# Kernel optimization log

Measured on AMD Instinct MI355X. Metric: run time of the kernel, lower is better.

The kernel has to match this reference:

```python
import jax, jax.numpy as jnp
import numpy as np

B, H, W, C = 4, 48, 48, 256
NQ = 8
NH = 8
FFN = 1024


def _dwconv(x, w, b):
    # x: (b,h,w,c); w: (kh,kw,1,c) depthwise; b: (c,)
    p = w.shape[0] // 2
    y = jax.lax.conv_general_dilated(
        x, w, (1, 1), [(p, p), (p, p)],
        dimension_numbers=('NHWC', 'HWIO', 'NHWC'),
        feature_group_count=x.shape[-1])
    return y + b


def _ln(x, g, b, eps=1e-6):
    m = jnp.mean(x, -1, keepdims=True)
    v = jnp.mean((x - m) ** 2, -1, keepdims=True)
    return (x - m) * jax.lax.rsqrt(v + eps) * g + b


def setup_inputs() -> dict:
    key = jax.random.key(0)
    ks = jax.random.split(key, 16)
    s = lambda k, sh, sc=0.02: jax.random.normal(k, sh, jnp.float32) * sc
    return dict(
        x=jax.random.normal(ks[0], (B, H, W, C), jnp.float32),
        queries=jax.random.normal(ks[1], (B, NQ, C), jnp.float32),
        epoch=10,
        pos_w=s(ks[2], (3, 3, 1, C)), pos_b=jnp.zeros((C,), jnp.float32),
        ln1_g=jnp.ones((C,), jnp.float32), ln1_b=jnp.zeros((C,), jnp.float32),
        q_w=s(ks[3], (C, C)), q_b=jnp.zeros((C,), jnp.float32),
        k_w=s(ks[4], (C, C)), k_b=jnp.zeros((C,), jnp.float32),
        v_w=s(ks[5], (C, C)), v_b=jnp.zeros((C,), jnp.float32),
        lepe_w=s(ks[6], (5, 5, 1, C)), lepe_b=jnp.zeros((C,), jnp.float32),
        out_w=s(ks[7], (C, C)), out_b=jnp.zeros((C,), jnp.float32),
        ln2_g=jnp.ones((C,), jnp.float32), ln2_b=jnp.zeros((C,), jnp.float32),
        fc1_w=s(ks[8], (FFN, C)), fc1_b=jnp.zeros((FFN,), jnp.float32),
        fc2_w=s(ks[9], (C, FFN)), fc2_b=jnp.zeros((C,), jnp.float32),
    )


def reference(x, queries, epoch, pos_w, pos_b, ln1_g, ln1_b,
              q_w, q_b, k_w, k_b, v_w, v_b, lepe_w, lepe_b,
              out_w, out_b, ln2_g, ln2_b, fc1_w, fc1_b, fc2_w, fc2_b):
    b, h, w, c = x.shape
    nq = queries.shape[1]
    N = nq + h * w

    # positional DWConv (3x3) residual
    x = x + _dwconv(x, pos_w, pos_b)
    xf = x.reshape(b, h * w, c)
    xq = jnp.concatenate([queries, xf], axis=1)  # (b, N, c)

    # region mask (epoch=10 -> soft softmax phase, tau exp-decayed)
    tau = 2.0 * (0.1 / 2.0) ** (epoch / 200.0)
    logits = jnp.einsum('bnc,bqc->bnq', xf, queries)  # (b, hw, nq)
    p = jax.nn.softmax(logits / tau, axis=-1)
    region = jnp.einsum('bik,bjk->bij', p, p)  # (b, hw, hw)
    mask = jnp.ones((b, N, N), x.dtype).at[:, nq:, nq:].set(region)

    # masked attention (faithful: v_h is built from scaled k, as in source)
    y = _ln(xq, ln1_g, ln1_b)
    q = y @ q_w.T + q_b
    k = y @ k_w.T + k_b
    v = y @ v_w.T + v_b
    lepe = _dwconv(v[:, nq:].reshape(b, h, w, -1), lepe_w, lepe_b).reshape(b, h * w, -1)
    k = k * (c // NH) ** -0.5
    qh = q.reshape(b, N, NH, -1).transpose(0, 2, 1, 3)  # (b, nh, N, d)
    kh = k.reshape(b, N, NH, -1).transpose(0, 2, 1, 3)
    vh = kh  # source assigns v_h from k
    qk = jnp.einsum('bhnd,bhmd->bhnm', qh, kh) * mask[:, None]
    att = jax.nn.softmax(qk, axis=-1)
    o = jnp.einsum('bhnm,bhmd->bhnd', att, vh)
    o = o.transpose(0, 2, 1, 3).reshape(b, N, -1)
    o = o.at[:, nq:, :].add(lepe)
    o = o @ out_w.T + out_b
    xq = xq + o

    # FFN
    z = _ln(xq, ln2_g, ln2_b)
    z = jax.nn.gelu(z @ fc1_w.T + fc1_b, approximate=False)
    z = z @ fc2_w.T + fc2_b
    xq = xq + z

    return xq[:, nq:, :].reshape(b, h, w, c), xq[:, :nq, :]
```

## Files before the change

kernel.cpp:

```cpp
#include <hip/hip_runtime.h>
#include <hip/hip_bf16.h>
#include <math.h>

typedef unsigned short u16;
constexpr int Bc = 4, Hc = 48, Wc = 48, Cc = 256;
constexpr int NQc = 8, HWc = 2304, Nc = 2312, NHc = 8, Dc = 32, FFNc = 1024;
constexpr int MRc = Bc * Nc;
constexpr int KTLDc = 2368;
constexpr float KSCALEc = 0.17677669529663687f;
constexpr float LOG2Ec  = 1.4426950408889634f;

typedef __attribute__((ext_vector_type(8))) short s8v;
typedef __attribute__((ext_vector_type(4))) float f32x4;

__device__ __forceinline__ u16 f2bf(float f) {
    union { __hip_bfloat16 h; u16 u; } c;
    c.h = __float2bfloat16(f);
    return c.u;
}
__device__ __forceinline__ float bf2f(u16 u) {
    return __uint_as_float(((unsigned)u) << 16);
}
__device__ __forceinline__ unsigned cvtpk2(float lo, float hi) {
    unsigned r;
    asm("v_cvt_pk_bf16_f32 %0, %1, %2" : "=v"(r) : "v"(lo), "v"(hi));
    return r;
}
__device__ __forceinline__ float fast_exp2(float x) {
    float r;
    asm("v_exp_f32 %0, %1" : "=v"(r) : "v"(x));
    return r;
}
__device__ __forceinline__ void gload16(const void* g, void* l) {
    __builtin_amdgcn_global_load_lds((const __attribute__((address_space(1))) void*)g,
                                     (__attribute__((address_space(3))) void*)l, 16, 0, 0);
}

__global__ __launch_bounds__(256) void fused_pre_kernel(
    const float* __restrict__ x, const float* __restrict__ queries, const int* __restrict__ epoch,
    const float* __restrict__ pos_w, const float* __restrict__ pos_b,
    const float* __restrict__ ln_g, const float* __restrict__ ln_b,
    const float* __restrict__ qw, const float* __restrict__ kw, const float* __restrict__ vw,
    const float* __restrict__ ow, const float* __restrict__ f1, const float* __restrict__ f2,
    float* __restrict__ xq, u16* __restrict__ ybf, u16* __restrict__ pbf,
    u16* __restrict__ wbf, u16* __restrict__ kt)
{
    int bi = blockIdx.x;
    if (bi >= 9248) {
        int bj = bi - 9248;
        if (bj < 768) {
            int i4 = bj * 256 + threadIdx.x;
            int idx = i4 * 4;
            const float* src; int off;
            if      (idx < 65536)  { src = qw; off = idx; }
            else if (idx < 131072) { src = kw; off = idx - 65536; }
            else if (idx < 196608) { src = vw; off = idx - 131072; }
            else if (idx < 262144) { src = ow; off = idx - 196608; }
            else if (idx < 524288) { src = f1; off = idx - 262144; }
            else                   { src = f2; off = idx - 524288; }
            float4 v = *(const float4*)(src + off);
            ushort4 o;
            o.x = f2bf(v.x); o.y = f2bf(v.y); o.z = f2bf(v.z); o.w = f2bf(v.w);
            *(ushort4*)(wbf + idx) = o;
        } else {
            int idx = (bj - 768) * 256 + threadIdx.x;
            if (idx < 1024 * 56) {
                int row = idx / 56, col = idx - row * 56;
                kt[(size_t)row * KTLDc + 2312 + col] = 0;
            }
        }
        return;
    }
    int blk = bi;
    int b = blk / Nc, n = blk - b * Nc;
    int c = threadIdx.x;
    bool sp = (n >= NQc);
    float val;
    if (sp) {
        int s = n - NQc;
        int hh = s / Wc, ww = s - hh * Wc;
        float acc = pos_b[c];
        float center = x[((b * Hc + hh) * Wc + ww) * Cc + c];
#pragma unroll
        for (int kh = 0; kh < 3; ++kh) {
            int yy = hh + kh - 1;
            if (yy < 0 || yy >= Hc) continue;
#pragma unroll
            for (int kw2 = 0; kw2 < 3; ++kw2) {
                int xx = ww + kw2 - 1;
                if (xx < 0 || xx >= Wc) continue;
                acc += x[((b * Hc + yy) * Wc + xx) * Cc + c] * pos_w[(kh * 3 + kw2) * Cc + c];
            }
        }
        val = center + acc;
    } else {
        val = queries[(b * NQc + n) * Cc + c];
    }
    xq[(size_t)blk * Cc + c] = val;

    float pq[8];
#pragma unroll
    for (int qi = 0; qi < 8; ++qi)
        pq[qi] = sp ? val * queries[(b * NQc + qi) * Cc + c] : 0.f;
    float r0 = val, r1 = val * val;
#pragma unroll
    for (int off = 32; off; off >>= 1) {
        r0 += __shfl_xor(r0, off);
        r1 += __shfl_xor(r1, off);
#pragma unroll
        for (int qi = 0; qi < 8; ++qi) pq[qi] += __shfl_xor(pq[qi], off);
    }
    __shared__ float red[4][10];
    __shared__ float fin[10];
    int wv = c >> 6, ln = c & 63;
    if (ln == 0) {
        red[wv][0] = r0; red[wv][1] = r1;
#pragma unroll
        for (int qi = 0; qi < 8; ++qi) red[wv][2 + qi] = pq[qi];
    }
    __syncthreads();
    if (c < 10) fin[c] = red[0][c] + red[1][c] + red[2][c] + red[3][c];
    __syncthreads();
    float mean = fin[0] * (1.0f / 256.0f);
    float var  = fin[1] * (1.0f / 256.0f) - mean * mean;
    float inv  = rsqrtf(var + 1e-6f);
    ybf[(size_t)blk * Cc + c] = f2bf((val - mean) * inv * ln_g[c] + ln_b[c]);

    if (sp && c < 8) {
        float it = 1.0f / (2.0f * powf(0.05f, (float)(*epoch) / 200.0f));
        float mx = -1e30f;
        float lg[8];
#pragma unroll
        for (int qi = 0; qi < 8; ++qi) { lg[qi] = fin[2 + qi] * it; mx = fmaxf(mx, lg[qi]); }
        float s = 0.f, mine = 0.f;
#pragma unroll
        for (int qi = 0; qi < 8; ++qi) {
            float ev = __expf(lg[qi] - mx);
            s += ev;
            if (qi == c) mine = ev;
        }
        pbf[((size_t)b * HWc + (n - NQc)) * 8 + c] = f2bf(mine / s);
    }
}

template <int ACT, int RESID, int OMODE>
__global__ __launch_bounds__(256) void mfma_gemm64_kernel(
    const u16* __restrict__ A, const u16* __restrict__ W,
    const float* __restrict__ bias, const float* resid,
    float* outF, u16* outB, int M, int N, int K, float scale)
{
    __shared__ u16 As[64 * 64];
    __shared__ u16 Bs[128 * 64];
    int t = threadIdx.x;
    int w = t >> 6, l = t & 63, lg = l >> 4, lr = l & 15;
    int wm = w >> 1, wn = w & 1;
    int m0 = blockIdx.y * 64, n0 = blockIdx.x * 128;
    f32x4 acc[2][4] = {};
    int lrow = l >> 3, lchunk = (l & 7) * 8;
    for (int k0 = 0; k0 < K; k0 += 64) {
        __syncthreads();
#pragma unroll
        for (int c = 0; c < 2; ++c) {
            int ar = m0 + w * 16 + c * 8 + lrow;
            if (ar >= M) ar = M - 1;
            gload16(A + (size_t)ar * K + k0 + lchunk, As + (w * 16 + c * 8) * 64);
        }
#pragma unroll
        for (int c = 0; c < 4; ++c) {
            int br = n0 + w * 32 + c * 8 + lrow;
            gload16(W + (size_t)br * K + k0 + lchunk, Bs + (w * 32 + c * 8) * 64);
        }
        __syncthreads();
#pragma unroll
        for (int kk = 0; kk < 64; kk += 32) {
            s8v aF[2], bF[4];
#pragma unroll
            for (int i = 0; i < 2; ++i)
                aF[i] = *(s8v*)&As[(wm * 32 + i * 16 + lr) * 64 + kk + lg * 8];
#pragma unroll
            for (int j = 0; j < 4; ++j)
                bF[j] = *(s8v*)&Bs[(wn * 64 + j * 16 + lr) * 64 + kk + lg * 8];
#pragma unroll
            for (int i = 0; i < 2; ++i)
#pragma unroll
                for (int j = 0; j < 4; ++j)
                    acc[i][j] = __builtin_amdgcn_mfma_f32_16x16x32_bf16(aF[i], bF[j], acc[i][j], 0, 0, 0);
        }
    }
#pragma unroll
    for (int j = 0; j < 4; ++j) {
        int n = n0 + wn * 64 + j * 16 + lr;
        float bv = bias[n];
#pragma unroll
        for (int i = 0; i < 2; ++i) {
#pragma unroll
            for (int r = 0; r < 4; ++r) {
                int m = m0 + wm * 32 + i * 16 + lg * 4 + r;
                if (m >= M) continue;
                float v = (acc[i][j][r] + bv) * scale;
                if (ACT == 1) {
                    float e = fast_exp2(2.302118f * (v + 0.044715f * v * v * v));
                    v = v * e * __builtin_amdgcn_rcpf(e + 1.0f);
                }
                if (RESID) v += resid[(size_t)m * N + n];
                if (OMODE == 0) {
                    outF[(size_t)m * N + n] = v;
                } else if (OMODE == 3) {
                    unsigned bb2 = (unsigned)m / 2312u;
                    unsigned tok = (unsigned)m - bb2 * 2312u;
                    size_t ob = (tok >= 8) ? (((size_t)(bb2 * 2304 + tok - 8)) << 8)
                                           : ((size_t)2359296 + (((size_t)(bb2 * 8 + tok)) << 8));
                    outF[ob + n] = v;
                } else {
                    outB[(size_t)m * N + n] = f2bf(v);
                }
            }
        }
    }
}

__global__ __launch_bounds__(256) void mfma_gemm_oln_kernel(
    const u16* __restrict__ A, const u16* __restrict__ V,
    const float* __restrict__ lw, const float* __restrict__ lbias,
    const u16* __restrict__ W, const float* __restrict__ bias,
    float* __restrict__ xq, const float* __restrict__ g, const float* __restrict__ bb,
    u16* __restrict__ ybf)
{
    const int K = Cc;
    constexpr int ALD = 264;
    __shared__ u16 As[32 * ALD];
    __shared__ u16 Bs[256 * 64];
    __shared__ float R[32][4][2];
    __shared__ float MI[32][2];
    int t = threadIdx.x;
    int w = t >> 6, l = t & 63, lg = l >> 4, lr = l & 15;
    int m0 = blockIdx.x * 32;
    int lrow = l >> 3, lchunk = (l & 7) * 8;

    for (int u = t; u < 1024; u += 256) {
        int row = u >> 5;
        int cg  = (u & 31) * 8;
        int m = m0 + row;
        int b2 = m / 2312, n = m - b2 * 2312;
        union { s8v s; u16 us[8]; } ov, res;
        ov.s = *(const s8v*)&A[(size_t)m * Cc + cg];
        if (n >= NQc) {
            int s0 = n - NQc, hh = s0 / Wc, ww = s0 - hh * Wc;
            float accv[8];
#pragma unroll
            for (int i = 0; i < 8; ++i) accv[i] = lbias[cg + i];
#pragma unroll
            for (int kh = 0; kh < 5; ++kh) {
                int yy = hh + kh - 2;
                if (yy < 0 || yy >= Hc) continue;
#pragma unroll
                for (int kw = 0; kw < 5; ++kw) {
                    int xx = ww + kw - 2;
                    if (xx < 0 || xx >= Wc) continue;
                    union { s8v s; u16 us[8]; } uv;
                    uv.s = *(const s8v*)&V[((size_t)b2 * Nc + NQc + yy * Wc + xx) * Cc + cg];
                    const float4* wp = (const float4*)&lw[(kh * 5 + kw) * Cc + cg];
                    float4 w0 = wp[0], w1 = wp[1];
                    accv[0] += bf2f(uv.us[0]) * w0.x;
                    accv[1] += bf2f(uv.us[1]) * w0.y;
                    accv[2] += bf2f(uv.us[2]) * w0.z;
                    accv[3] += bf2f(uv.us[3]) * w0.w;
                    accv[4] += bf2f(uv.us[4]) * w1.x;
                    accv[5] += bf2f(uv.us[5]) * w1.y;
                    accv[6] += bf2f(uv.us[6]) * w1.z;
                    accv[7] += bf2f(uv.us[7]) * w1.w;
                }
            }
#pragma unroll
            for (int i = 0; i < 8; ++i) res.us[i] = f2bf(bf2f(ov.us[i]) + accv[i]);
        } else {
            res.s = ov.s;
        }
        *(s8v*)&As[row * ALD + cg] = res.s;
    }

    f32x4 acc[2][4] = {};
    for (int k0 = 0; k0 < K; k0 += 64) {
        __syncthreads();
#pragma unroll
        for (int c = 0; c < 8; ++c)
            gload16(W + (size_t)(w * 64 + c * 8 + lrow) * K + k0 + lchunk, Bs + (w * 64 + c * 8) * 64);
        __syncthreads();
#pragma unroll
        for (int kk = 0; kk < 64; kk += 32) {
            s8v aF[2], bF[4];
#pragma unroll
            for (int i = 0; i < 2; ++i)
                aF[i] = *(s8v*)&As[(i * 16 + lr) * ALD + k0 + kk + lg * 8];
#pragma unroll
            for (int j = 0; j < 4; ++j)
                bF[j] = *(s8v*)&Bs[(w * 64 + j * 16 + lr) * 64 + kk + lg * 8];
#pragma unroll
            for (int i = 0; i < 2; ++i)
#pragma unroll
                for (int j = 0; j < 4; ++j)
                    acc[i][j] = __builtin_amdgcn_mfma_f32_16x16x32_bf16(aF[i], bF[j], acc[i][j], 0, 0, 0);
        }
    }
    float s[2][4], ss[2][4];
#pragma unroll
    for (int i = 0; i < 2; ++i)
#pragma unroll
        for (int r = 0; r < 4; ++r) { s[i][r] = 0.f; ss[i][r] = 0.f; }
#pragma unroll
    for (int j = 0; j < 4; ++j) {
        int n = w * 64 + j * 16 + lr;
        float bv = bias[n];
#pragma unroll
        for (int i = 0; i < 2; ++i) {
#pragma unroll
            for (int r = 0; r < 4; ++r) {
                int m = m0 + i * 16 + lg * 4 + r;
                float v = acc[i][j][r] + bv + xq[(size_t)m * Cc + n];
                acc[i][j][r] = v;
                xq[(size_t)m * Cc + n] = v;
                s[i][r] += v;
                ss[i][r] += v * v;
            }
        }
    }
#pragma unroll
    for (int i = 0; i < 2; ++i)
#pragma unroll
        for (int r = 0; r < 4; ++r) {
#pragma unroll
            for (int off = 1; off < 16; off <<= 1) {
                s[i][r]  += __shfl_xor(s[i][r], off);
                ss[i][r] += __shfl_xor(ss[i][r], off);
            }
        }
    __syncthreads();
    if (lr == 0) {
#pragma unroll
        for (int i = 0; i < 2; ++i)
#pragma unroll
            for (int r = 0; r < 4; ++r) {
                int row = i * 16 + lg * 4 + r;
                R[row][w][0] = s[i][r];
                R[row][w][1] = ss[i][r];
            }
    }
    __syncthreads();
    if (t < 32) {
        float tot  = R[t][0][0] + R[t][1][0] + R[t][2][0] + R[t][3][0];
        float tots = R[t][0][1] + R[t][1][1] + R[t][2][1] + R[t][3][1];
        float mean = tot * (1.0f / 256.0f);
        float var  = tots * (1.0f / 256.0f) - mean * mean;
        MI[t][0] = mean;
        MI[t][1] = rsqrtf(var + 1e-6f);
    }
    __syncthreads();
#pragma unroll
    for (int j = 0; j < 4; ++j) {
        int n = w * 64 + j * 16 + lr;
        float gv = g[n], bbv = bb[n];
#pragma unroll
        for (int i = 0; i < 2; ++i) {
#pragma unroll
            for (int r = 0; r < 4; ++r) {
                int row = i * 16 + lg * 4 + r;
                float mean = MI[row][0], inv = MI[row][1];
                int m = m0 + row;
                ybf[(size_t)m * Cc + n] = f2bf((acc[i][j][r] - mean) * inv * gv + bbv);
            }
        }
    }
}

__global__ __launch_bounds__(256) void mfma_gemm_qkv64_kernel(
    const u16* __restrict__ A, const u16* __restrict__ W,
    const float* __restrict__ q_b, const float* __restrict__ k_b, const float* __restrict__ v_b,
    u16* __restrict__ outq, u16* __restrict__ outk, u16* __restrict__ outkt, u16* __restrict__ outv)
{
    const int M = MRc, K = Cc;
    __shared__ u16 As[64 * 64];
    __shared__ u16 Bs[128 * 64];
    int t = threadIdx.x;
    int w = t >> 6, l = t & 63, lg = l >> 4, lr = l & 15;
    int wm = w >> 1, wn = w & 1;
    int m0 = blockIdx.y * 64, n0 = blockIdx.x * 128;
    int range = n0 >> 8;
    f32x4 acc[2][4] = {};
    int lrow = l >> 3, lchunk = (l & 7) * 8;
    for (int k0 = 0; k0 < K; k0 += 64) {
        __syncthreads();
#pragma unroll
        for (int c = 0; c < 2; ++c) {
            int ar = m0 + w * 16 + c * 8 + lrow;
            if (ar >= M) ar = M - 1;
            gload16(A + (size_t)ar * K + k0 + lchunk, As + (w * 16 + c * 8) * 64);
        }
#pragma unroll
        for (int c = 0; c < 4; ++c) {
            int br = n0 + w * 32 + c * 8 + lrow;
            gload16(W + (size_t)br * K + k0 + lchunk, Bs + (w * 32 + c * 8) * 64);
        }
        __syncthreads();
#pragma unroll
        for (int kk = 0; kk < 64; kk += 32) {
            s8v aF[2], bF[4];
#pragma unroll
            for (int i = 0; i < 2; ++i)
                aF[i] = *(s8v*)&As[(wm * 32 + i * 16 + lr) * 64 + kk + lg * 8];
#pragma unroll
            for (int j = 0; j < 4; ++j)
                bF[j] = *(s8v*)&Bs[(wn * 64 + j * 16 + lr) * 64 + kk + lg * 8];
#pragma unroll
            for (int i = 0; i < 2; ++i)
#pragma unroll
                for (int j = 0; j < 4; ++j)
                    acc[i][j] = __builtin_amdgcn_mfma_f32_16x16x32_bf16(aF[i], bF[j], acc[i][j], 0, 0, 0);
        }
    }
    const float* bias = (range == 0) ? q_b : (range == 1) ? k_b : v_b;
    u16* dst = (range == 0) ? outq : (range == 1) ? outk : outv;
    float scale = (range == 0) ? LOG2Ec : (range == 1) ? KSCALEc : 1.0f;
#pragma unroll
    for (int j = 0; j < 4; ++j) {
        int n = n0 + wn * 64 + j * 16 + lr;
        int nc = n & 255;
        float bv = bias[nc];
#pragma unroll
        for (int i = 0; i < 2; ++i) {
#pragma unroll
            for (int r = 0; r < 4; ++r) {
                int m = m0 + wm * 32 + i * 16 + lg * 4 + r;
                if (m >= M) continue;
                float v = (acc[i][j][r] + bv) * scale;
                u16 hv = f2bf(v);
                dst[(size_t)m * 256 + nc] = hv;
                if (range == 1) {
                    unsigned um = (unsigned)m;
                    unsigned bb = um / 2312u;
                    unsigned nr = um - bb * 2312u;
                    outkt[((size_t)(bb * NHc + (nc >> 5)) * Dc + (nc & 31)) * KTLDc + nr] = hv;
                }
            }
        }
    }
}

__global__ __launch_bounds__(256, 4) void attn_mfma_kernel(const u16* __restrict__ q,
                                                           const u16* __restrict__ k,
                                                           const u16* __restrict__ kt,
                                                           const u16* __restrict__ p,
                                                           u16* __restrict__ o)
{
    constexpr int KT = 64;
    constexpr int NT = (Nc + KT - 1) / KT;
    __shared__ __align__(16) u16 Kls[KT * 40];
    __shared__ __align__(16) u16 Ktls[32 * 88];
    __shared__ __align__(16) unsigned PW[4][16 * 36];

    int flat = blockIdx.x;
    int grp  = flat & 31;
    int qblk = flat >> 5;
    int b = grp >> 3, h = grp & 7;

    int t = threadIdx.x;
    int w = t >> 6, l = t & 63, lg = l >> 4, lr = l & 15;
    int q0 = qblk * 64 + w * 16;

    int qrow = q0 + lr;
    bool qtok = (qrow < NQc);
    int qrc = qrow < Nc ? qrow : Nc - 1;
    s8v qB = *(const s8v*)&q[((size_t)b * Nc + qrc) * Cc + h * Dc + lg * 8];

    s8v pqB = {0, 0, 0, 0, 0, 0, 0, 0};
    if (lg == 0 && qrow >= NQc && qrow < Nc)
        pqB = *(const s8v*)&p[((size_t)b * HWc + (qrow - NQc)) * 8];

    f32x4 accO[2] = {{0.f, 0.f, 0.f, 0.f}, {0.f, 0.f, 0.f, 0.f}};
    float lrun = 0.f;

    int srow = t >> 2, sseg = (t & 3) * 8;
    int td = t >> 3, tks = (t & 7) * 8;
    const u16* ktbase = kt + ((size_t)(b * NHc + h) * Dc + td) * KTLDc;
    const u16* pbase  = p + (size_t)b * HWc * 8;
    unsigned* PWr = &PW[w][lr * 36];
    int bsrc = lg * 20;

    s8v kv8 = {0,0,0,0,0,0,0,0};
    if (srow < Nc)
        kv8 = *(const s8v*)&k[((size_t)b * Nc + srow) * Cc + h * Dc + sseg];
    s8v kt8 = *(const s8v*)&ktbase[tks];

    for (int ti = 0; ti < NT; ++ti) {
        int m0 = ti * KT;
        bool tail = (ti == NT - 1);
        __syncthreads();
        *(s8v*)&Kls[srow * 40 + sseg] = kv8;
        *(s8v*)&Ktls[td * 88 + tks]   = kt8;
        __syncthreads();

        if (ti + 1 < NT) {
            int n0g = m0 + KT;
            kv8 = (s8v){0,0,0,0,0,0,0,0};
            int kvg = n0g + srow;
            if (kvg < Nc)
                kv8 = *(const s8v*)&k[((size_t)b * Nc + kvg) * Cc + h * Dc + sseg];
            kt8 = *(const s8v*)&ktbase[n0g + tks];
        }

        float sc[4][4];
#pragma unroll
        for (int cb = 0; cb < 4; ++cb) {
            s8v kA = *(s8v*)&Kls[(cb * 16 + lr) * 40 + lg * 8];
            f32x4 St = __builtin_amdgcn_mfma_f32_16x16x32_bf16(kA, qB, (f32x4){0.f,0.f,0.f,0.f}, 0, 0, 0);
            s8v pkA = {0, 0, 0, 0, 0, 0, 0, 0};
            if (lg == 0) {
                int kvr = m0 + cb * 16 + lr;
                if (kvr >= NQc && kvr < Nc)
                    pkA = *(const s8v*)&pbase[(size_t)(kvr - NQc) * 8];
            }
            f32x4 Mv = __builtin_amdgcn_mfma_f32_16x16x32_bf16(pkA, pqB, (f32x4){0.f,0.f,0.f,0.f}, 0, 0, 0);
            bool ktok = (ti == 0 && cb == 0 && lg < 2);
#pragma unroll
            for (int j = 0; j < 4; ++j) {
                float mval = (qtok || ktok) ? 1.f : Mv[j];
                sc[cb][j] = St[j] * mval;
            }
        }
        float tsum = 0.f;
#pragma unroll
        for (int cb = 0; cb < 4; ++cb)
#pragma unroll
            for (int j = 0; j < 4; ++j) {
                float ev = fast_exp2(sc[cb][j]);
                if (tail && (cb != 0 || lg >= 2)) ev = 0.f;
                sc[cb][j] = ev;
                tsum += ev;
            }
        tsum += __shfl_xor(tsum, 16);
        tsum += __shfl_xor(tsum, 32);
        lrun += tsum;
#pragma unroll
        for (int cb = 0; cb < 4; ++cb) {
            uint2 pk2;
            pk2.x = cvtpk2(sc[cb][0], sc[cb][1]);
            pk2.y = cvtpk2(sc[cb][2], sc[cb][3]);
            *(uint2*)&PWr[8 * cb + 2 * lg] = pk2;
        }
#pragma unroll
        for (int kc = 0; kc < 2; ++kc) {
            s8v pA = *(s8v*)&PWr[16 * kc + 4 * lg];
#pragma unroll
            for (int db = 0; db < 2; ++db) {
                s8v vB = *(s8v*)&Ktls[(db * 16 + lr) * 88 + kc * 32 + lg * 8];
                accO[db] = __builtin_amdgcn_mfma_f32_16x16x32_bf16(pA, vB, accO[db], 0, 0, 0);
            }
        }
    }

    float lb[4];
#pragma unroll
    for (int j = 0; j < 4; ++j) lb[j] = __shfl(lrun, bsrc + j);
#pragma unroll
    for (int db = 0; db < 2; ++db)
#pragma unroll
        for (int j = 0; j < 4; ++j) {
            int rowg = q0 + lg * 4 + j;
            if (rowg < Nc)
                o[((size_t)b * Nc + rowg) * Cc + h * Dc + db * 16 + lr] = f2bf(accO[db][j] / lb[j]);
        }
}

extern "C" void kernel_launch(void* const* d_in, const int* in_sizes, int n_in,
                              void* d_out, int out_size, void* d_ws, size_t ws_size,
                              hipStream_t stream)
{
    const float* x       = (const float*)d_in[0];
    const float* queries = (const float*)d_in[1];
    const int*   epoch   = (const int*)d_in[2];
    const float* pos_w   = (const float*)d_in[3];
    const float* pos_b   = (const float*)d_in[4];
    const float* ln1_g   = (const float*)d_in[5];
    const float* ln1_b   = (const float*)d_in[6];
    const float* q_w     = (const float*)d_in[7];
    const float* q_b     = (const float*)d_in[8];
    const float* k_w     = (const float*)d_in[9];
    const float* k_b     = (const float*)d_in[10];
    const float* v_w     = (const float*)d_in[11];
    const float* v_b     = (const float*)d_in[12];
    const float* lepe_w  = (const float*)d_in[13];
    const float* lepe_b  = (const float*)d_in[14];
    const float* out_w   = (const float*)d_in[15];
    const float* out_b   = (const float*)d_in[16];
    const float* ln2_g   = (const float*)d_in[17];
    const float* ln2_b   = (const float*)d_in[18];
    const float* fc1_w   = (const float*)d_in[19];
    const float* fc1_b   = (const float*)d_in[20];
    const float* fc2_w   = (const float*)d_in[21];
    const float* fc2_b   = (const float*)d_in[22];

    float* ws = (float*)d_ws;
    float* xq  = ws;
    u16*  ybf  = (u16*)(ws + 2367488);
    u16*  qbf  = (u16*)(ws + 3551232);
    u16*  kbf  = (u16*)(ws + 4734976);
    u16*  ktbf = (u16*)(ws + 5918720);
    u16*  pbf  = (u16*)(ws + 7131136);
    u16*  obf  = (u16*)(ws + 7168000);
    u16*  vbf  = (u16*)(ws + 8351744);
    u16*  wbf  = (u16*)(ws + 9535488);
    u16*  ffn  = qbf;

    u16* w_o  = wbf + 196608;
    u16* w_f1 = wbf + 262144;
    u16* w_f2 = wbf + 524288;

    fused_pre_kernel<<<9248 + 768 + 224, 256, 0, stream>>>(
        x, queries, epoch, pos_w, pos_b, ln1_g, ln1_b,
        q_w, k_w, v_w, out_w, fc1_w, fc2_w,
        xq, ybf, pbf, wbf, ktbf);

    mfma_gemm_qkv64_kernel<<<dim3(6, 145), 256, 0, stream>>>(ybf, wbf, q_b, k_b, v_b, qbf, kbf, ktbf, vbf);

    attn_mfma_kernel<<<1184, 256, 0, stream>>>(qbf, kbf, ktbf, pbf, obf);

    mfma_gemm_oln_kernel<<<289, 256, 0, stream>>>(obf, vbf, lepe_w, lepe_b,
                                                  w_o, out_b, xq, ln2_g, ln2_b, ybf);

    mfma_gemm64_kernel<1,0,1><<<dim3(8, 145), 256, 0, stream>>>(ybf, w_f1, fc1_b, nullptr, nullptr, ffn, MRc, 1024, 256, 1.0f);
    mfma_gemm64_kernel<0,1,3><<<dim3(2, 145), 256, 0, stream>>>(ffn, w_f2, fc2_b, xq, (float*)d_out, nullptr, MRc, 256, 1024, 1.0f);
}
```

Baseline: 225.0 us.

## Move LePE depthwise conv into extra blocks of attention kernel

The 5x5 depthwise LePE convolution is moved out of the output-projection GEMM's A-tile staging. It now runs in 1152 extra blocks appended to the attention launch, which write a bf16 lepe buffer. The GEMM then just loads and adds that buffer. The aim is to overlap the conv with attention and shorten the serial prologue of the 289-block GEMM, at the cost of an extra global write and read of the lepe tensor plus extra blocks competing with attention for occupancy.

```diff
diff --git a/kernel.cpp b/kernel.cpp
--- a/kernel.cpp
+++ b/kernel.cpp
@@ -220,8 +220,7 @@
 }
 
 __global__ __launch_bounds__(256) void mfma_gemm_oln_kernel(
-    const u16* __restrict__ A, const u16* __restrict__ V,
-    const float* __restrict__ lw, const float* __restrict__ lbias,
+    const u16* __restrict__ A, const u16* __restrict__ L,
     const u16* __restrict__ W, const float* __restrict__ bias,
     float* __restrict__ xq, const float* __restrict__ g, const float* __restrict__ bb,
     u16* __restrict__ ybf)
@@ -245,34 +244,10 @@
         union { s8v s; u16 us[8]; } ov, res;
         ov.s = *(const s8v*)&A[(size_t)m * Cc + cg];
         if (n >= NQc) {
-            int s0 = n - NQc, hh = s0 / Wc, ww = s0 - hh * Wc;
-            float accv[8];
-#pragma unroll
-            for (int i = 0; i < 8; ++i) accv[i] = lbias[cg + i];
-#pragma unroll
-            for (int kh = 0; kh < 5; ++kh) {
-                int yy = hh + kh - 2;
-                if (yy < 0 || yy >= Hc) continue;
-#pragma unroll
-                for (int kw = 0; kw < 5; ++kw) {
-                    int xx = ww + kw - 2;
-                    if (xx < 0 || xx >= Wc) continue;
-                    union { s8v s; u16 us[8]; } uv;
-                    uv.s = *(const s8v*)&V[((size_t)b2 * Nc + NQc + yy * Wc + xx) * Cc + cg];
-                    const float4* wp = (const float4*)&lw[(kh * 5 + kw) * Cc + cg];
-                    float4 w0 = wp[0], w1 = wp[1];
-                    accv[0] += bf2f(uv.us[0]) * w0.x;
-                    accv[1] += bf2f(uv.us[1]) * w0.y;
-                    accv[2] += bf2f(uv.us[2]) * w0.z;
-                    accv[3] += bf2f(uv.us[3]) * w0.w;
-                    accv[4] += bf2f(uv.us[4]) * w1.x;
-                    accv[5] += bf2f(uv.us[5]) * w1.y;
-                    accv[6] += bf2f(uv.us[6]) * w1.z;
-                    accv[7] += bf2f(uv.us[7]) * w1.w;
-                }
-            }
-#pragma unroll
-            for (int i = 0; i < 8; ++i) res.us[i] = f2bf(bf2f(ov.us[i]) + accv[i]);
+            union { s8v s; u16 us[8]; } lv;
+            lv.s = *(const s8v*)&L[((size_t)b2 * HWc + (n - NQc)) * Cc + cg];
+#pragma unroll
+            for (int i = 0; i < 8; ++i) res.us[i] = f2bf(bf2f(ov.us[i]) + bf2f(lv.us[i]));
         } else {
             res.s = ov.s;
         }
@@ -449,7 +424,11 @@
                                                            const u16* __restrict__ k,
                                                            const u16* __restrict__ kt,
                                                            const u16* __restrict__ p,
-                                                           u16* __restrict__ o)
+                                                           u16* __restrict__ o,
+                                                           const u16* __restrict__ v,
+                                                           const float* __restrict__ lw,
+                                                           const float* __restrict__ lbias,
+                                                           u16* __restrict__ lepebf)
 {
     constexpr int KT = 64;
     constexpr int NT = (Nc + KT - 1) / KT;
@@ -458,6 +437,46 @@
     __shared__ __align__(16) unsigned PW[4][16 * 36];
 
     int flat = blockIdx.x;
+    if (flat >= 1184) {
+        int idx = (flat - 1184) * 256 + threadIdx.x;
+        int cg = (idx & 31) * 8;
+        int sp = idx >> 5;
+        int ww = sp % Wc;
+        int t2 = sp / Wc;
+        int hh = t2 % Hc;
+        int b  = t2 / Hc;
+        float acc[8];
+#pragma unroll
+        for (int i = 0; i < 8; ++i) acc[i] = lbias[cg + i];
+#pragma unroll
+        for (int kh = 0; kh < 5; ++kh) {
+            int yy = hh + kh - 2;
+            if (yy < 0 || yy >= Hc) continue;
+#pragma unroll
+            for (int kw = 0; kw < 5; ++kw) {
+                int xx = ww + kw - 2;
+                if (xx < 0 || xx >= Wc) continue;
+                union { s8v s; u16 u[8]; } uv;
+                uv.s = *(const s8v*)&v[((size_t)b * Nc + NQc + yy * Wc + xx) * Cc + cg];
+                const float4* wp = (const float4*)&lw[(kh * 5 + kw) * Cc + cg];
+                float4 w0 = wp[0], w1 = wp[1];
+                acc[0] += bf2f(uv.u[0]) * w0.x;
+                acc[1] += bf2f(uv.u[1]) * w0.y;
+                acc[2] += bf2f(uv.u[2]) * w0.z;
+                acc[3] += bf2f(uv.u[3]) * w0.w;
+                acc[4] += bf2f(uv.u[4]) * w1.x;
+                acc[5] += bf2f(uv.u[5]) * w1.y;
+                acc[6] += bf2f(uv.u[6]) * w1.z;
+                acc[7] += bf2f(uv.u[7]) * w1.w;
+            }
+        }
+        union { s8v s; u16 u[8]; } res;
+#pragma unroll
+        for (int i = 0; i < 8; ++i) res.u[i] = f2bf(acc[i]);
+        *(s8v*)&lepebf[((size_t)t2 * Wc + ww) * Cc + cg] = res.s;
+        return;
+    }
+
     int grp  = flat & 31;
     int qblk = flat >> 5;
     int b = grp >> 3, h = grp & 7;
@@ -608,6 +627,7 @@
     u16*  obf  = (u16*)(ws + 7168000);
     u16*  vbf  = (u16*)(ws + 8351744);
     u16*  wbf  = (u16*)(ws + 9535488);
+    u16*  lepebf = (u16*)(ws + 9928704);
     u16*  ffn  = qbf;
 
     u16* w_o  = wbf + 196608;
@@ -621,10 +641,10 @@
 
     mfma_gemm_qkv64_kernel<<<dim3(6, 145), 256, 0, stream>>>(ybf, wbf, q_b, k_b, v_b, qbf, kbf, ktbf, vbf);
 
-    attn_mfma_kernel<<<1184, 256, 0, stream>>>(qbf, kbf, ktbf, pbf, obf);
-
-    mfma_gemm_oln_kernel<<<289, 256, 0, stream>>>(obf, vbf, lepe_w, lepe_b,
-                                                  w_o, out_b, xq, ln2_g, ln2_b, ybf);
+    attn_mfma_kernel<<<1184 + 1152, 256, 0, stream>>>(qbf, kbf, ktbf, pbf, obf,
+                                                      vbf, lepe_w, lepe_b, lepebf);
+
+    mfma_gemm_oln_kernel<<<289, 256, 0, stream>>>(obf, lepebf, w_o, out_b, xq, ln2_g, ln2_b, ybf);
 
     mfma_gemm64_kernel<1,0,1><<<dim3(8, 145), 256, 0, stream>>>(ybf, w_f1, fc1_b, nullptr, nullptr, ffn, MRc, 1024, 256, 1.0f);
     mfma_gemm64_kernel<0,1,3><<<dim3(2, 145), 256, 0, stream>>>(ffn, w_f2, fc2_b, xq, (float*)d_out, nullptr, MRc, 256, 1024, 1.0f);
```

Result: faster. 194.7 us (-13.5%).
